# Optimization experiments

Measured on AMD Instinct MI355X. Metric: run time of the kernel, lower is better.

The kernel has to match this reference:

```python
import jax, jax.numpy as jnp
import numpy as np

DEPTH = 256
SEQ = 394
EMB = 300


def _branch(x_nch, W, b, n):
    # W: [depth, n*EMB], flatten order of paragraph[i:i+n,:].flatten() is (time, emb)
    k = W.reshape(DEPTH, n, EMB).transpose(0, 2, 1)  # OIH: [depth, EMB, n]
    y = jax.lax.conv_general_dilated(
        x_nch, k, window_strides=(1,), padding='VALID',
        dimension_numbers=('NCH', 'OIH', 'NCH'))  # [B, depth, SEQ-n+1]
    # original loop only covers windows i = 0 .. SEQ-n-1 (SEQ-n windows)
    y = y[:, :, :SEQ - n] + b  # b: [depth, 1] broadcasts over time
    # running max starts at 0 and relu clamps >= 0; outer relu is a no-op
    return jnp.max(jax.nn.relu(y), axis=-1)  # [B, depth]


def setup_inputs() -> dict:
    key = jax.random.key(0)
    ks = jax.random.split(key, 7)
    inp = {
        'input': jax.random.normal(ks[0], (64, SEQ, EMB), dtype=jnp.float32),
        'W1': jax.random.normal(ks[1], (DEPTH, 3 * EMB), dtype=jnp.float32),
        'W2': jax.random.normal(ks[2], (DEPTH, 4 * EMB), dtype=jnp.float32),
        'W3': jax.random.normal(ks[3], (DEPTH, 5 * EMB), dtype=jnp.float32),
        'b1': jax.random.normal(ks[4], (DEPTH, 1), dtype=jnp.float32),
        'b2': jax.random.normal(ks[5], (DEPTH, 1), dtype=jnp.float32),
        'b3': jax.random.normal(ks[6], (DEPTH, 1), dtype=jnp.float32),
    }
    return inp


def reference(input, W1, W2, W3, b1, b2, b3):
    x = input.transpose(0, 2, 1)  # [B, EMB, SEQ] (NCH)
    o1 = _branch(x, W1, b1, 3)
    o2 = _branch(x, W2, b2, 4)
    o3 = _branch(x, W3, b3, 5)
    return jnp.concatenate([o1, o2, o3], axis=1)  # [B, 3*depth]
```

## Files before the change

### kernel.cpp

```cpp
#include <hip/hip_runtime.h>
#include <hip/hip_bf16.h>

#define SEQ 394
#define EMB 300
#define EMBP 312
#define NROWS (64 * SEQ)
#define NCHT 118
#define CBE0 29
#define CBE1 68
#define RPB 128
#define NBLK 197
#define XROWS 132
#define XGR 5148
#define XELEM 41184

typedef __attribute__((ext_vector_type(8))) short short8;
typedef __attribute__((ext_vector_type(4))) float f32x4;

__device__ __forceinline__ unsigned short f2b(float f) {
    unsigned u = __float_as_uint(f);
    u += 0x7FFFu + ((u >> 16) & 1u);
    return (unsigned short)(u >> 16);
}


__global__ __launch_bounds__(256)
void pack_w_kernel(const float* __restrict__ W1, const float* __restrict__ W2,
                   const float* __restrict__ W3, unsigned short* __restrict__ wb)
{
    int G = blockIdx.x * 256 + threadIdx.x;
    int l  = G & 63;
    int g  = (G >> 6) & 15;
    int c  = G >> 10;
    const float* Wg; int n, cb;
    if (c <= CBE0)      { Wg = W1; n = 3; cb = 0;        }
    else if (c <= CBE1) { Wg = W2; n = 4; cb = CBE0 + 1; }
    else                { Wg = W3; n = 5; cb = CBE1 + 1; }
    const int K = n * 300;
    const int f = g * 16 + (l & 15);
    const int kl = (c - cb) * 32 + (l >> 4) * 8;
    unsigned short v[8];
#pragma unroll
    for (int j = 0; j < 8; ++j) {
        int kk = kl + j;
        int r  = kk / EMBP;
        int e  = kk - r * EMBP;
        v[j] = (r < n && e < 300) ? f2b(Wg[(long)f * K + r * 300 + e]) : (unsigned short)0;
    }
    unsigned short* dst = wb + (long)G * 8;
    *(ushort4*)dst       = make_ushort4(v[0], v[1], v[2], v[3]);
    *(ushort4*)(dst + 4) = make_ushort4(v[4], v[5], v[6], v[7]);
}


__global__ __launch_bounds__(1024, 1)
void convgemm_kernel(const float* __restrict__ x,
                     const unsigned short* __restrict__ wb,
                     const float* __restrict__ b1, const float* __restrict__ b2,
                     const float* __restrict__ b3,
                     float* __restrict__ out)
{
    __shared__ unsigned short X[XELEM];

    const int tid  = threadIdx.x;
    const int lane = tid & 63;
    const int wid  = tid >> 6;
    const int wfs  = wid >> 1;
    const int ws   = wid & 1;
    const int lr   = lane & 15, lg = lane >> 4;
    const long r0  = (long)blockIdx.x * RPB;

    const unsigned short* wp0 = wb + ((long)(wfs * 2) * 64 + lane) * 8;
    auto LDW = [&](int c, short8 (&w)[2]) {
        const short8* p = (const short8*)(wp0 + (long)c * 8192);
        w[0] = p[0];
        w[1] = p[64];
    };

    short8 w1[2], w2[2];
    LDW(30, w1); LDW(69, w2);

    {
        const float* xs = x + r0 * 300;
#pragma unroll
        for (int rd = 0; rd < 6; ++rd) {
            int gi = rd * 1024 + tid;
            if (gi < XGR) {
                int row = gi / 39;
                int g   = gi - row * 39;
                const float* src = xs + (long)gi * 8 - 12 * row;
                float4 v0 = make_float4(0.f, 0.f, 0.f, 0.f);
                float4 v1 = make_float4(0.f, 0.f, 0.f, 0.f);
                if (r0 + row < NROWS) {
                    if (g < 37) {
                        v0 = *(const float4*)src;
                        v1 = *(const float4*)(src + 4);
                    } else if (g == 37) {
                        v0 = *(const float4*)src;
                    }
                }
                short8 s;
                s[0] = (short)f2b(v0.x); s[1] = (short)f2b(v0.y);
                s[2] = (short)f2b(v0.z); s[3] = (short)f2b(v0.w);
                s[4] = (short)f2b(v1.x); s[5] = (short)f2b(v1.y);
                s[6] = (short)f2b(v1.z); s[7] = (short)f2b(v1.w);
                *(short8*)&X[gi * 8] = s;
            }
        }
    }
    __syncthreads();

    const unsigned short* xr = &X[(ws * 64 + lr) * EMBP + lg * 8];
    auto RDBX = [&](int ko, short8 (&bx)[4]) {
        bx[0] = *(const short8*)(xr + ko);
        bx[1] = *(const short8*)(xr + ko + 16 * EMBP);
        bx[2] = *(const short8*)(xr + ko + 32 * EMBP);
        bx[3] = *(const short8*)(xr + ko + 48 * EMBP);
    };

    auto MFMA8 = [&](const short8 (&w)[2], const short8 (&bx)[4], f32x4 (&acc)[2][4]) {
#pragma unroll
        for (int mi = 0; mi < 2; ++mi)
#pragma unroll
            for (int ni = 0; ni < 4; ++ni)
                acc[mi][ni] = __builtin_amdgcn_mfma_f32_16x16x32_bf16(w[mi], bx[ni], acc[mi][ni], 0, 0, 0);
    };

    const int  B0  = (int)(r0 / SEQ);
    const long rB1 = (long)(B0 + 1) * SEQ;
    const bool cross = (r0 + RPB - 1) >= rB1;

    auto EPI = [&](int br, f32x4 (&acc)[2][4]) {
        const float* bg = (br == 0) ? b1 : (br == 1) ? b2 : b3;
        const int Nw = 391 - br;
#pragma unroll
        for (int mi = 0; mi < 2; ++mi) {
#pragma unroll
            for (int r = 0; r < 4; ++r) {
                const int d = wfs * 32 + mi * 16 + lg * 4 + r;
                const float bv = bg[d];
                float vlo = 0.f, vhi = 0.f;
#pragma unroll
                for (int ni = 0; ni < 4; ++ni) {
                    long rr = r0 + ws * 64 + ni * 16 + lr;
                    bool hi = rr >= rB1;
                    long ii = rr - (hi ? rB1 : (long)B0 * SEQ);
                    float v = fmaxf(acc[mi][ni][r] + bv, 0.f);
                    if (ii >= Nw) v = 0.f;
                    vlo = hi ? vlo : fmaxf(vlo, v);
                    vhi = hi ? fmaxf(vhi, v) : vhi;
                }
#pragma unroll
                for (int off = 1; off < 16; off <<= 1) {
                    vlo = fmaxf(vlo, __shfl_xor(vlo, off));
                    vhi = fmaxf(vhi, __shfl_xor(vhi, off));
                }
                if (lr == 0) {
                    atomicMax((int*)(out + (long)B0 * 768 + br * 256 + d), __float_as_int(vlo));
                    if (cross && B0 + 1 < 64)
                        atomicMax((int*)(out + (long)(B0 + 1) * 768 + br * 256 + d), __float_as_int(vhi));
                }
            }
        }
#pragma unroll
        for (int i = 0; i < 2; ++i)
#pragma unroll
            for (int j = 0; j < 4; ++j)
                acc[i][j] = (f32x4)0.0f;
    };

    f32x4 accA[2][4], accB[2][4];
#pragma unroll
    for (int i = 0; i < 2; ++i)
#pragma unroll
        for (int j = 0; j < 4; ++j) {
            accA[i][j] = (f32x4)0.0f;
            accB[i][j] = (f32x4)0.0f;
        }

    short8 bxA[4], bxB[4];
    RDBX(0, bxA);

    for (int j = 0; j < 38; j += 2) {
        RDBX((j + 1) * 32, bxB);
        MFMA8(w1, bxA, accA);
        MFMA8(w2, bxA, accB);
        LDW(30 + j + 1, w1); LDW(69 + j + 1, w2);

        RDBX((j + 2) * 32, bxA);
        MFMA8(w1, bxB, accA);
        MFMA8(w2, bxB, accB);
        LDW(30 + j + 2, w1); LDW(69 + j + 2, w2);
    }
    MFMA8(w1, bxA, accA);
    MFMA8(w2, bxA, accB);

    LDW(108, w2);
    RDBX(39 * 32, bxB);
    EPI(1, accA);

    for (int u = 0; u < 10; u += 2) {
        RDBX((40 + u) * 32, bxA);
        MFMA8(w2, bxB, accB);
        LDW(109 + u, w2);

        { int t = (41 + u <= 48) ? 41 + u : 48; RDBX(t * 32, bxB); }
        MFMA8(w2, bxA, accB);
        { int t = (110 + u <= 117) ? 110 + u : 117; LDW(t, w2); }
    }

    LDW(0, w1);
    RDBX(0, bxA);
    EPI(2, accB);

    for (int j = 0; j < 30; j += 2) {
        RDBX((j + 1) * 32, bxB);
        MFMA8(w1, bxA, accA);
        LDW(j + 1, w1);

        { int t = (j + 2 <= 29) ? j + 2 : 29; RDBX(t * 32, bxA); }
        MFMA8(w1, bxB, accA);
        { int t = (j + 2 <= 29) ? j + 2 : 29; LDW(t, w1); }
    }
    EPI(0, accA);
}


__device__ __forceinline__ void load_chunk(const float* __restrict__ Wg,
                                           const float* __restrict__ xb,
                                           int K, int dbase, int i0, int k0, int tid,
                                           float4 wv[4], float4 xv[4])
{
#pragma unroll
    for (int i = 0; i < 4; ++i) {
        int fi  = tid + (i << 8);
        int row = fi >> 3;
        int c4  = (fi & 7) << 2;
        int col = k0 + c4;
        if (col < K)
            wv[i] = *(const float4*)(Wg + (long)(dbase + row) * K + col);
        else
            wv[i] = make_float4(0.f, 0.f, 0.f, 0.f);
        int off = (i0 + row) * EMB + col;
        int lim = SEQ * EMB - 4;
        if (off > lim) off = lim;
        xv[i] = *(const float4*)(xb + off);
    }
}

__device__ __forceinline__ void write_chunk(unsigned short (*Wb)[40],
                                            unsigned short (*Xb)[40],
                                            int tid, const float4 wv[4], const float4 xv[4])
{
#pragma unroll
    for (int i = 0; i < 4; ++i) {
        int fi  = tid + (i << 8);
        int row = fi >> 3;
        int c4  = (fi & 7) << 2;
        *(ushort4*)&Wb[row][c4] = make_ushort4(f2b(wv[i].x), f2b(wv[i].y), f2b(wv[i].z), f2b(wv[i].w));
        *(ushort4*)&Xb[row][c4] = make_ushort4(f2b(xv[i].x), f2b(xv[i].y), f2b(xv[i].z), f2b(xv[i].w));
    }
}

__global__ __launch_bounds__(256, 2)
void convmax_fallback(const float* __restrict__ x,
                      const float* __restrict__ W1, const float* __restrict__ W2,
                      const float* __restrict__ W3,
                      const float* __restrict__ b1, const float* __restrict__ b2,
                      const float* __restrict__ b3,
                      float* __restrict__ out)
{
    const int br = blockIdx.z;
    const int K  = (br == 0) ? 900 : (br == 1) ? 1200 : 1500;
    const int Nw = SEQ - 3 - br;
    const float* Wg = (br == 0) ? W1 : (br == 1) ? W2 : W3;
    const float* bg = (br == 0) ? b1 : (br == 1) ? b2 : b3;
    const int b  = blockIdx.x;
    const int mt = blockIdx.y >> 2;
    const int nt = blockIdx.y & 3;
    const int dbase = mt * 128;
    const int i0    = nt * 128;
    const float* xb = x + b * (SEQ * EMB);
    const int nch = (K + 31) >> 5;

    __shared__ unsigned short Wl[2][128][40];
    __shared__ unsigned short Xl[2][128][40];

    const int tid  = threadIdx.x;
    const int lane = tid & 63;
    const int wid  = tid >> 6;
    const int wr = wid >> 1, wc = wid & 1;
    const int lr = lane & 15, lg = lane >> 4;

    f32x4 acc[4][4];
#pragma unroll
    for (int i = 0; i < 4; ++i)
#pragma unroll
        for (int j = 0; j < 4; ++j)
            acc[i][j] = (f32x4)0.0f;

    {
        float4 wv[4], xv[4];
        load_chunk(Wg, xb, K, dbase, i0, 0, tid, wv, xv);
        write_chunk(Wl[0], Xl[0], tid, wv, xv);
    }
    __syncthreads();

    for (int c = 0; c < nch; ++c) {
        const int cur = c & 1;
        float4 wv[4], xv[4];
        const bool pf = (c + 1 < nch);
        if (pf) load_chunk(Wg, xb, K, dbase, i0, (c + 1) << 5, tid, wv, xv);

        short8 af[4], bfr[4];
#pragma unroll
        for (int mi = 0; mi < 4; ++mi)
            af[mi] = *(const short8*)&Wl[cur][wr * 64 + mi * 16 + lr][lg * 8];
#pragma unroll
        for (int ni = 0; ni < 4; ++ni)
            bfr[ni] = *(const short8*)&Xl[cur][wc * 64 + ni * 16 + lr][lg * 8];
#pragma unroll
        for (int mi = 0; mi < 4; ++mi)
#pragma unroll
            for (int ni = 0; ni < 4; ++ni)
                acc[mi][ni] = __builtin_amdgcn_mfma_f32_16x16x32_bf16(af[mi], bfr[ni], acc[mi][ni], 0, 0, 0);

        if (pf) write_chunk(Wl[cur ^ 1], Xl[cur ^ 1], tid, wv, xv);
        __syncthreads();
    }

    const int ob = b * 768 + br * 256;
#pragma unroll
    for (int mi = 0; mi < 4; ++mi) {
#pragma unroll
        for (int rI = 0; rI < 4; ++rI) {
            const int d = dbase + wr * 64 + mi * 16 + lg * 4 + rI;
            const float bv = bg[d];
            float m = 0.f;
#pragma unroll
            for (int ni = 0; ni < 4; ++ni) {
                int win = i0 + wc * 64 + ni * 16 + lr;
                float v = acc[mi][ni][rI] + bv;
                v = fmaxf(v, 0.f);
                if (win >= Nw) v = 0.f;
                m = fmaxf(m, v);
            }
#pragma unroll
            for (int off = 1; off < 16; off <<= 1)
                m = fmaxf(m, __shfl_xor(m, off));
            if (lr == 0)
                atomicMax((int*)(out + ob + d), __float_as_int(m));
        }
    }
}


extern "C" void kernel_launch(void* const* d_in, const int* in_sizes, int n_in,
                              void* d_out, int out_size, void* d_ws, size_t ws_size,
                              hipStream_t stream) {
    const float* x  = (const float*)d_in[0];
    const float* W1 = (const float*)d_in[1];
    const float* W2 = (const float*)d_in[2];
    const float* W3 = (const float*)d_in[3];
    const float* b1 = (const float*)d_in[4];
    const float* b2 = (const float*)d_in[5];
    const float* b3 = (const float*)d_in[6];
    float* out = (float*)d_out;

    hipMemsetAsync(d_out, 0, (size_t)out_size * sizeof(float), stream);

    const size_t need = (size_t)NCHT * 8192 * 2;

    if (ws_size >= need) {
        unsigned short* wbb = (unsigned short*)d_ws;
        pack_w_kernel<<<472, 256, 0, stream>>>(W1, W2, W3, wbb);
        convgemm_kernel<<<NBLK, 1024, 0, stream>>>(x, wbb, b1, b2, b3, out);
    } else {
        dim3 grid(64, 8, 3);
        convmax_fallback<<<grid, 256, 0, stream>>>(x, W1, W2, W3, b1, b2, b3, out);
    }
}
```

Baseline: 76.40 us.

## Switch conv GEMM to 32x32x16 MFMA tiles with 512-thread blocks

Replaces the 16x16x32 bf16 MFMA tiling with 32x32x16 MFMAs, repacking the weight layout and the LDS read pattern so each wave owns a 64-filter by 64-row tile. Blocks shrink from 1024 to 512 threads (8 waves) with two blocks allowed per CU, and the epilogue reduction widens to 32 lanes. The goal is fewer MFMA issues and fewer LDS reads per unit of work, plus more overlap between the two co-resident blocks. In exchange each wave holds larger accumulators and weight fragments, which raises register pressure. Per-wave work doubles, and the incomplete view leaves it unclear whether the unseen later branch loops were adapted to the new tiling.

```diff
diff --git a/kernel.cpp b/kernel.cpp
--- a/kernel.cpp
+++ b/kernel.cpp
@@ -10,12 +10,12 @@
 #define CBE1 68
 #define RPB 128
 #define NBLK 197
-#define XROWS 132
 #define XGR 5148
 #define XELEM 41184
 
 typedef __attribute__((ext_vector_type(8))) short short8;
 typedef __attribute__((ext_vector_type(4))) float f32x4;
+typedef __attribute__((ext_vector_type(16))) float f32x16;
 
 __device__ __forceinline__ unsigned short f2b(float f) {
     unsigned u = __float_as_uint(f);
@@ -30,15 +30,16 @@
 {
     int G = blockIdx.x * 256 + threadIdx.x;
     int l  = G & 63;
-    int g  = (G >> 6) & 15;
+    int ks = (G >> 6) & 1;
+    int g  = (G >> 7) & 7;
     int c  = G >> 10;
     const float* Wg; int n, cb;
     if (c <= CBE0)      { Wg = W1; n = 3; cb = 0;        }
     else if (c <= CBE1) { Wg = W2; n = 4; cb = CBE0 + 1; }
     else                { Wg = W3; n = 5; cb = CBE1 + 1; }
     const int K = n * 300;
-    const int f = g * 16 + (l & 15);
-    const int kl = (c - cb) * 32 + (l >> 4) * 8;
+    const int f = g * 32 + (l & 31);
+    const int kl = (c - cb) * 32 + ks * 16 + (l >> 5) * 8;
     unsigned short v[8];
 #pragma unroll
     for (int j = 0; j < 8; ++j) {
@@ -53,7 +54,7 @@
 }
 
 
-__global__ __launch_bounds__(1024, 1)
+__global__ __launch_bounds__(512, 2)
 void convgemm_kernel(const float* __restrict__ x,
                      const unsigned short* __restrict__ wb,
                      const float* __restrict__ b1, const float* __restrict__ b2,
@@ -67,24 +68,27 @@
     const int wid  = tid >> 6;
     const int wfs  = wid >> 1;
     const int ws   = wid & 1;
-    const int lr   = lane & 15, lg = lane >> 4;
+    const int lm   = lane & 31;
+    const int l5   = lane >> 5;
     const long r0  = (long)blockIdx.x * RPB;
 
-    const unsigned short* wp0 = wb + ((long)(wfs * 2) * 64 + lane) * 8;
-    auto LDW = [&](int c, short8 (&w)[2]) {
+    const unsigned short* wp0 = wb + ((long)(wfs * 2) * 128 + lane) * 8;
+    auto LDW = [&](int c, short8 (&w)[4]) {
         const short8* p = (const short8*)(wp0 + (long)c * 8192);
         w[0] = p[0];
         w[1] = p[64];
+        w[2] = p[128];
+        w[3] = p[192];
     };
 
-    short8 w1[2], w2[2];
+    short8 w1[4], w2[4];
     LDW(30, w1); LDW(69, w2);
 
     {
         const float* xs = x + r0 * 300;
 #pragma unroll
-        for (int rd = 0; rd < 6; ++rd) {
-            int gi = rd * 1024 + tid;
+        for (int rd = 0; rd < 11; ++rd) {
+            int gi = rd * 512 + tid;
             if (gi < XGR) {
                 int row = gi / 39;
                 int g   = gi - row * 39;
@@ -110,52 +114,54 @@
     }
     __syncthreads();
 
-    const unsigned short* xr = &X[(ws * 64 + lr) * EMBP + lg * 8];
+    const unsigned short* xr = &X[(ws * 64 + lm) * EMBP + l5 * 8];
     auto RDBX = [&](int ko, short8 (&bx)[4]) {
         bx[0] = *(const short8*)(xr + ko);
-        bx[1] = *(const short8*)(xr + ko + 16 * EMBP);
-        bx[2] = *(const short8*)(xr + ko + 32 * EMBP);
-        bx[3] = *(const short8*)(xr + ko + 48 * EMBP);
+        bx[1] = *(const short8*)(xr + ko + 16);
+        bx[2] = *(const short8*)(xr + 32 * EMBP + ko);
+        bx[3] = *(const short8*)(xr + 32 * EMBP + ko + 16);
     };
 
-    auto MFMA8 = [&](const short8 (&w)[2], const short8 (&bx)[4], f32x4 (&acc)[2][4]) {
-#pragma unroll
-        for (int mi = 0; mi < 2; ++mi)
-#pragma unroll
-            for (int ni = 0; ni < 4; ++ni)
-                acc[mi][ni] = __builtin_amdgcn_mfma_f32_16x16x32_bf16(w[mi], bx[ni], acc[mi][ni], 0, 0, 0);
+    auto MFMA8 = [&](const short8 (&w)[4], const short8 (&bx)[4], f32x16 (&acc)[2][2]) {
+#pragma unroll
+        for (int mt = 0; mt < 2; ++mt)
+#pragma unroll
+            for (int nt = 0; nt < 2; ++nt) {
+                acc[mt][nt] = __builtin_amdgcn_mfma_f32_32x32x16_bf16(w[mt * 2],     bx[nt * 2],     acc[mt][nt], 0, 0, 0);
+                acc[mt][nt] = __builtin_amdgcn_mfma_f32_32x32x16_bf16(w[mt * 2 + 1], bx[nt * 2 + 1], acc[mt][nt], 0, 0, 0);
+            }
     };
 
     const int  B0  = (int)(r0 / SEQ);
     const long rB1 = (long)(B0 + 1) * SEQ;
     const bool cross = (r0 + RPB - 1) >= rB1;
 
-    auto EPI = [&](int br, f32x4 (&acc)[2][4]) {
+    auto EPI = [&](int br, f32x16 (&acc)[2][2]) {
         const float* bg = (br == 0) ? b1 : (br == 1) ? b2 : b3;
         const int Nw = 391 - br;
 #pragma unroll
-        for (int mi = 0; mi < 2; ++mi) {
-#pragma unroll
-            for (int r = 0; r < 4; ++r) {
-                const int d = wfs * 32 + mi * 16 + lg * 4 + r;
+        for (int mt = 0; mt < 2; ++mt) {
+#pragma unroll
+            for (int r = 0; r < 16; ++r) {
+                const int d = wfs * 64 + mt * 32 + (r & 3) + 8 * (r >> 2) + 4 * l5;
                 const float bv = bg[d];
                 float vlo = 0.f, vhi = 0.f;
 #pragma unroll
-                for (int ni = 0; ni < 4; ++ni) {
-                    long rr = r0 + ws * 64 + ni * 16 + lr;
+                for (int nt = 0; nt < 2; ++nt) {
+                    long rr = r0 + ws * 64 + nt * 32 + lm;
                     bool hi = rr >= rB1;
                     long ii = rr - (hi ? rB1 : (long)B0 * SEQ);
-                    float v = fmaxf(acc[mi][ni][r] + bv, 0.f);
+                    float v = fmaxf(acc[mt][nt][r] + bv, 0.f);
                     if (ii >= Nw) v = 0.f;
                     vlo = hi ? vlo : fmaxf(vlo, v);
                     vhi = hi ? fmaxf(vhi, v) : vhi;
                 }
 #pragma unroll
-                for (int off = 1; off < 16; off <<= 1) {
+                for (int off = 1; off < 32; off <<= 1) {
                     vlo = fmaxf(vlo, __shfl_xor(vlo, off));
                     vhi = fmaxf(vhi, __shfl_xor(vhi, off));
                 }
-                if (lr == 0) {
+                if (lm == 0) {
                     atomicMax((int*)(out + (long)B0 * 768 + br * 256 + d), __float_as_int(vlo));
                     if (cross && B0 + 1 < 64)
                         atomicMax((int*)(out + (long)(B0 + 1) * 768 + br * 256 + d), __float_as_int(vhi));
@@ -165,17 +171,17 @@
 #pragma unroll
         for (int i = 0; i < 2; ++i)
 #pragma unroll
-            for (int j = 0; j < 4; ++j)
-                acc[i][j] = (f32x4)0.0f;
+            for (int j = 0; j < 2; ++j)
+                acc[i][j] = (f32x16)0.0f;
     };
 
-    f32x4 accA[2][4], accB[2][4];
+    f32x16 accA[2][2], accB[2][2];
 #pragma unroll
     for (int i = 0; i < 2; ++i)
 #pragma unroll
-        for (int j = 0; j < 4; ++j) {
-            accA[i][j] = (f32x4)0.0f;
-            accB[i][j] = (f32x4)0.0f;
+        for (int j = 0; j < 2; ++j) {
+            accA[i][j] = (f32x16)0.0f;
+            accB[i][j] = (f32x16)0.0f;
         }
 
     short8 bxA[4], bxB[4];
@@ -374,7 +380,7 @@
     if (ws_size >= need) {
         unsigned short* wbb = (unsigned short*)d_ws;
         pack_w_kernel<<<472, 256, 0, stream>>>(W1, W2, W3, wbb);
-        convgemm_kernel<<<NBLK, 1024, 0, stream>>>(x, wbb, b1, b2, b3, out);
+        convgemm_kernel<<<NBLK, 512, 0, stream>>>(x, wbb, b1, b2, b3, out);
     } else {
         dim3 grid(64, 8, 3);
         convmax_fallback<<<grid, 256, 0, stream>>>(x, W1, W2, W3, b1, b2, b3, out);
```

Result: slower. 126.9 us (+66.0%).
